# Performance work log

Measured on AMD Instinct MI355X. Metric: run time of the kernel, lower is better.

Reference implementation:

```python
import jax, jax.numpy as jnp
import numpy as np

EPS = 1e-6
ROPE_THETA = 1000000.0

def _rmsnorm(x, scale):
    var = jnp.mean(jnp.square(x), axis=-1, keepdims=True)
    return x * jax.lax.rsqrt(var + EPS) * scale

def _rope(x, positions):
    # x: [B, h, T, H]; GPT-NeoX style rotate-half
    H = x.shape[-1]
    half = H // 2
    inv_freq = 1.0 / (ROPE_THETA ** (jnp.arange(half, dtype=jnp.float32) * 2.0 / H))
    ang = positions.astype(jnp.float32)[:, None] * inv_freq[None, :]  # [T, half]
    cos, sin = jnp.cos(ang), jnp.sin(ang)
    x1, x2 = x[..., :half], x[..., half:]
    return jnp.concatenate([x1 * cos - x2 * sin, x2 * cos + x1 * sin], axis=-1)

def setup_inputs() -> dict:
    key = jax.random.key(0)
    ks = jax.random.split(key, 16)
    B, T, D = 2, 2048, 2048
    N, K, H = 16, 2, 128
    I = 5504
    s = 0.02
    return {
        "x": jax.random.normal(ks[0], (B, T, D), jnp.float32),
        "positions": jnp.arange(T, dtype=jnp.int32),
        "ln1_scale": jnp.ones((D,), jnp.float32),
        "q_w": jax.random.normal(ks[1], (N, D, H), jnp.float32) * s,
        "q_b": jax.random.normal(ks[2], (N, H), jnp.float32) * s,
        "k_w": jax.random.normal(ks[3], (K, D, H), jnp.float32) * s,
        "k_b": jax.random.normal(ks[4], (K, H), jnp.float32) * s,
        "v_w": jax.random.normal(ks[5], (K, D, H), jnp.float32) * s,
        "v_b": jax.random.normal(ks[6], (K, H), jnp.float32) * s,
        "o_w": jax.random.normal(ks[7], (N, H, D), jnp.float32) * s,
        "ln2_scale": jnp.ones((D,), jnp.float32),
        "gate_w": jax.random.normal(ks[8], (D, I), jnp.float32) * s,
        "up_w": jax.random.normal(ks[9], (D, I), jnp.float32) * s,
        "down_w": jax.random.normal(ks[10], (I, D), jnp.float32) * s,
    }

def reference(x, positions, ln1_scale, q_w, q_b, k_w, k_b, v_w, v_b, o_w,
              ln2_scale, gate_w, up_w, down_w):
    B, T, D = x.shape
    N, _, H = q_w.shape
    K = k_w.shape[0]
    group = N // K

    h = _rmsnorm(x, ln1_scale)

    # Projections (per source einsums) + bias
    q = jnp.einsum('btd,ndh->bnth', h, q_w) + q_b[None, :, None, :]
    k = jnp.einsum('btd,kdh->bkth', h, k_w) + k_b[None, :, None, :]
    v = jnp.einsum('btd,kdh->bkth', h, v_w) + v_b[None, :, None, :]

    q = _rope(q, positions) * (H ** -0.5)
    k = _rope(k, positions)

    # GQA: expand kv heads to query heads
    k = jnp.repeat(k, group, axis=1)  # [B,N,T,H]
    v = jnp.repeat(v, group, axis=1)

    # Causal self-attention (prefill path: kv cache filled from k, v)
    scores = jnp.einsum('bnth,bnsh->bnts', q, k)
    causal = positions[:, None] >= positions[None, :]  # [T, T]
    scores = jnp.where(causal[None, None, :, :], scores, -jnp.inf)
    probs = jax.nn.softmax(scores, axis=-1)
    attn = jnp.einsum('bnts,bnsh->bnth', probs, v)

    o = jnp.einsum('bnth,nhd->btd', attn, o_w)

    # Residual + post-attn norm + SwiGLU MLP + residual
    res = o + x
    h2 = _rmsnorm(res, ln2_scale)
    fuse = jax.nn.silu(h2 @ gate_w) * (h2 @ up_w)
    return res + fuse @ down_w
```

## Files before the change

### kernel.cpp

```cpp
#include <hip/hip_runtime.h>
#include <cstdint>
#include <cstddef>

typedef unsigned short u16;
typedef __attribute__((ext_vector_type(8))) short short8;
typedef __attribute__((ext_vector_type(4))) float f32x4;

#define DEV __device__ __forceinline__

DEV float bf2f(u16 v) { union { unsigned u; float f; } x; x.u = ((unsigned)v) << 16; return x.f; }
DEV u16 f2bf(float f) {
  union { float f; unsigned u; } x; x.f = f;
  unsigned r = x.u + 0x7fffu + ((x.u >> 16) & 1u);
  return (u16)(r >> 16);
}

DEV void gload_lds16(const void* g, void* l) {
  __builtin_amdgcn_global_load_lds((const __attribute__((address_space(1))) void*)g,
                                   (__attribute__((address_space(3))) void*)l, 16, 0, 0);
}

#define BARRIER __builtin_amdgcn_s_barrier()
#define VM0 asm volatile("s_waitcnt vmcnt(0)" ::: "memory")
#define VM4 asm volatile("s_waitcnt vmcnt(4)" ::: "memory")

DEV void rmsnorm_row(const float* __restrict__ x, const float* __restrict__ scale,
                     u16* __restrict__ out, int row, int tid, float* red)
{
  const float* xr = x + (size_t)row * 2048;
  const float4 v0 = *(const float4*)&xr[tid * 8];
  const float4 v1 = *(const float4*)&xr[tid * 8 + 4];
  float ss = v0.x * v0.x + v0.y * v0.y + v0.z * v0.z + v0.w * v0.w +
             v1.x * v1.x + v1.y * v1.y + v1.z * v1.z + v1.w * v1.w;
#pragma unroll
  for (int d = 32; d > 0; d >>= 1) ss += __shfl_down(ss, d);
  if ((tid & 63) == 0) red[tid >> 6] = ss;
  __syncthreads();
  const float tot = red[0] + red[1] + red[2] + red[3];
  const float inv = rsqrtf(tot * (1.f / 2048.f) + 1e-6f);
  const float* sc = scale + tid * 8;
  short8 ov;
  ov[0] = (short)f2bf(v0.x * inv * sc[0]); ov[1] = (short)f2bf(v0.y * inv * sc[1]);
  ov[2] = (short)f2bf(v0.z * inv * sc[2]); ov[3] = (short)f2bf(v0.w * inv * sc[3]);
  ov[4] = (short)f2bf(v1.x * inv * sc[4]); ov[5] = (short)f2bf(v1.y * inv * sc[5]);
  ov[6] = (short)f2bf(v1.z * inv * sc[6]); ov[7] = (short)f2bf(v1.w * inv * sc[7]);
  *(short8*)&out[(size_t)row * 2048 + tid * 8] = ov;
}

DEV void transpose_tile(const float* __restrict__ in, u16* __restrict__ out,
                        int R, int C, int mode, int bx, int by, int bz,
                        int tid, float (&tile)[64][65])
{
  const int tx = tid & 31, ty = tid >> 5;
  const int c0 = bx * 64, r0 = by * 64;
  const float* inb = in + (size_t)bz * R * C;
  u16* outb = out + (size_t)bz * R * C;
#pragma unroll
  for (int i = 0; i < 8; ++i) {
    const int r = ty + i * 8;
    const float2 v = *(const float2*)&inb[(size_t)(r0 + r) * C + c0 + tx * 2];
    tile[r][tx * 2] = v.x;
    tile[r][tx * 2 + 1] = v.y;
  }
  __syncthreads();
#pragma unroll
  for (int i = 0; i < 8; ++i) {
    const int jj = ty + i * 8;
    const int j = c0 + jj;
    const int prow = mode ? ((j >> 7) * 256 + (((j >> 5) & 3) << 6) + ((mode == 2) << 5) + (j & 31))
                          : j;
    const unsigned a = f2bf(tile[tx * 2][jj]);
    const unsigned b = f2bf(tile[tx * 2 + 1][jj]);
    *(unsigned*)&outb[(size_t)prow * R + r0 + tx * 2] = a | (b << 16);
  }
}

__global__ __launch_bounds__(256) void prep_kernel(
    const float* __restrict__ q_w, const float* __restrict__ k_w,
    const float* __restrict__ v_w, const float* __restrict__ o_w,
    const float* __restrict__ gate_w, const float* __restrict__ up_w,
    const float* __restrict__ down_w,
    const float* __restrict__ qb, const float* __restrict__ kb,
    const float* __restrict__ vb,
    const float* __restrict__ x, const float* __restrict__ ln1,
    u16* __restrict__ wqkv_t, u16* __restrict__ o_wt,
    u16* __restrict__ gu_t, u16* __restrict__ d_t, float* __restrict__ bias,
    u16* __restrict__ hbuf)
{
  __shared__ float tile[64][65];
  const int bid = (int)blockIdx.x;
  const int tid = threadIdx.x;
  if (bid < 1024) {
    transpose_tile(q_w, wqkv_t, 2048, 128, 0, bid & 1, (bid >> 1) & 31, bid >> 6, tid, tile);
  } else if (bid < 1152) {
    const int l = bid - 1024;
    transpose_tile(k_w, wqkv_t + 2048LL * 2048, 2048, 128, 0, l & 1, (l >> 1) & 31, l >> 6, tid, tile);
  } else if (bid < 1280) {
    const int l = bid - 1152;
    transpose_tile(v_w, wqkv_t + 2304LL * 2048, 2048, 128, 0, l & 1, (l >> 1) & 31, l >> 6, tid, tile);
  } else if (bid < 2304) {
    const int l = bid - 1280;
    transpose_tile(o_w, o_wt, 2048, 2048, 0, l & 31, l >> 5, 0, tid, tile);
  } else if (bid < 5056) {
    const int l = bid - 2304;
    transpose_tile(gate_w, gu_t, 2048, 5504, 1, l % 86, l / 86, 0, tid, tile);
  } else if (bid < 7808) {
    const int l = bid - 5056;
    transpose_tile(up_w, gu_t, 2048, 5504, 2, l % 86, l / 86, 0, tid, tile);
  } else if (bid < 10560) {
    const int l = bid - 7808;
    transpose_tile(down_w, d_t, 5504, 2048, 0, l & 31, l >> 5, 0, tid, tile);
  } else if (bid < 10570) {
    const int i = (bid - 10560) * 256 + tid;
    if (i < 2048) bias[i] = qb[i];
    else if (i < 2304) bias[i] = kb[i - 2048];
    else if (i < 2560) bias[i] = vb[i - 2304];
  } else {
    rmsnorm_row(x, ln1, hbuf, bid - 10570, tid, &tile[0][0]);
  }
}

__global__ __launch_bounds__(256) void rmsnorm_kernel(
    const float* __restrict__ x, const float* __restrict__ scale, u16* __restrict__ out)
{
  __shared__ float red[4];
  rmsnorm_row(x, scale, out, blockIdx.x, threadIdx.x, red);
}

template <int BM, int BN, int TB, int MODE, int GR>
__global__ __launch_bounds__(TB, 512 / TB) void gemm_conv_kernel(
    const u16* __restrict__ A, const u16* __restrict__ Bt,
    void* C, const float* __restrict__ aux, int N, int K, int lda, int ldb)
{
  constexpr int MFRAG = BM / 32;
  constexpr int AISS = BM * 8 / TB;
  constexpr int BISS = BN * 8 / TB;
  constexpr int WN = BN / 64;
  __shared__ __align__(16) u16 As[2][BM * 64];
  __shared__ __align__(16) u16 Bs[3][BN * 64];

  const int tid = threadIdx.x;
  const int wv = tid >> 6, lane = tid & 63, lo = lane & 15, hi = lane >> 4;
  const int wm = wv / WN, wn = wv % WN;

  const int nwg = (int)gridDim.x;
  const int id0 = (int)blockIdx.x;
  const int id = (id0 & 7) * (nwg >> 3) + (id0 >> 3);
  const int ncol = N / BN;
  const int rg = id % GR, cc = (id / GR) % ncol, gg = id / (GR * ncol);
  const int by = gg * GR + rg, bx = cc;
  const int row0 = by * BM, col0 = bx * BN;

  const f32x4 fz = {0.f, 0.f, 0.f, 0.f};
  f32x4 acc[MFRAG][4];
#pragma unroll
  for (int m = 0; m < MFRAG; ++m)
#pragma unroll
    for (int n = 0; n < 4; ++n) acc[m][n] = fz;

  const int nt = K >> 6;

  auto STAGE_A = [&](int kt, int ab) {
#pragma unroll
    for (int i = 0; i < AISS; ++i) {
      const int f = i * TB + tid;
      const int rp = f >> 3, sp = tid & 7;
      gload_lds16(A + (size_t)(row0 + rp) * lda + kt * 64 + ((sp ^ (rp & 7)) * 8),
                  (char*)&As[ab][0] + (i * TB + wv * 64) * 16);
    }
  };
  auto STAGE_B = [&](int kt, int bb) {
#pragma unroll
    for (int i = 0; i < BISS; ++i) {
      const int f = i * TB + tid;
      const int rp = f >> 3, sp = tid & 7;
      gload_lds16(Bt + (size_t)(col0 + rp) * ldb + kt * 64 + ((sp ^ (rp & 7)) * 8),
                  (char*)&Bs[bb][0] + (i * TB + wv * 64) * 16);
    }
  };

#define LDA8M(ARR, BUF, S, G)                                                    \
  _Pragma("unroll")                                                              \
  for (int mt = 0; mt < 4; ++mt) {                                               \
    const int r = wm * (BM / 2) + ((G) * 4 + mt) * 16 + lo;                      \
    ARR[mt] = *(const short8*)&As[BUF][r * 64 + (((S) * 4 + hi) ^ (r & 7)) * 8]; \
  }
#define LDB8M(ARR, BUF, S)                                                       \
  _Pragma("unroll")                                                              \
  for (int nn = 0; nn < 4; ++nn) {                                               \
    const int r = wn * 64 + nn * 16 + lo;                                        \
    ARR[nn] = *(const short8*)&Bs[BUF][r * 64 + (((S) * 4 + hi) ^ (r & 7)) * 8]; \
  }
#define MFMA16M(AR, BR, G)                                                       \
  __builtin_amdgcn_s_setprio(1);                                                 \
  _Pragma("unroll")                                                              \
  for (int mt = 0; mt < 4; ++mt)                                                 \
    _Pragma("unroll")                                                            \
    for (int nn = 0; nn < 4; ++nn)                                               \
      acc[(G) * 4 + mt][nn] = __builtin_amdgcn_mfma_f32_16x16x32_bf16(           \
          AR[mt], BR[nn], acc[(G) * 4 + mt][nn], 0, 0, 0);                       \
  __builtin_amdgcn_s_setprio(0);

  STAGE_A(0, 0); STAGE_B(0, 0); STAGE_B(1, 1);
  VM4; BARRIER;

  int ab = 0, bcur = 0;
  for (int t = 0; t < nt; ++t) {
    const bool preA = (t + 1 < nt);
    const bool preB = (t + 2 < nt);
    const int bs2 = (bcur >= 1) ? bcur - 1 : 2;
    if constexpr (BM == 256) {
      short8 a0[4], a1[4], b0[4], a2[4], a3[4], b1[4];
      LDA8M(a0, ab, 0, 0); LDA8M(a1, ab, 0, 1); LDB8M(b0, bcur, 0);
      LDA8M(a2, ab, 1, 0); LDA8M(a3, ab, 1, 1); LDB8M(b1, bcur, 1);
      if (preA) STAGE_A(t + 1, ab ^ 1);
      if (preB) STAGE_B(t + 2, bs2);
      MFMA16M(a0, b0, 0); MFMA16M(a1, b0, 1);
      MFMA16M(a2, b1, 0); MFMA16M(a3, b1, 1);
      if (preA) { if (preB) VM4; else VM0; }
      BARRIER;
    } else {
      short8 a0[4], b0[4], a1[4], b1[4];
      LDA8M(a0, ab, 0, 0); LDB8M(b0, bcur, 0);
      LDA8M(a1, ab, 1, 0); LDB8M(b1, bcur, 1);
      if (preA) STAGE_A(t + 1, ab ^ 1);
      if (preB) STAGE_B(t + 2, bs2);
      MFMA16M(a0, b0, 0);
      MFMA16M(a1, b1, 0);
      if (preA) { if (preB) VM4; else VM0; }
      BARRIER;
    }
    ab ^= 1;
    bcur = (bcur == 2) ? 0 : bcur + 1;
  }
#undef LDA8M
#undef LDB8M
#undef MFMA16M

  float* Cf = (float*)C;
  u16* Ch = (u16*)C;
  if constexpr (MODE == 4) {
    const int ldo = N >> 1;
#pragma unroll
    for (int fm = 0; fm < MFRAG; ++fm) {
#pragma unroll
      for (int nn = 0; nn < 2; ++nn) {
        const int fcol = (col0 >> 1) + wn * 32 + nn * 16 + lo;
#pragma unroll
        for (int j = 0; j < 4; ++j) {
          const int row = row0 + wm * (BM / 2) + fm * 16 + hi * 4 + j;
          const float g = acc[fm][nn][j];
          const float u = acc[fm][nn + 2][j];
          const float sg = g / (1.f + __builtin_amdgcn_exp2f(-1.4426950408889634f * g));
          Ch[(size_t)row * ldo + fcol] = f2bf(sg * u);
        }
      }
    }
  } else {
#pragma unroll
    for (int fm = 0; fm < MFRAG; ++fm) {
#pragma unroll
      for (int nn = 0; nn < 4; ++nn) {
        const int col = col0 + wn * 64 + nn * 16 + lo;
#pragma unroll
        for (int j = 0; j < 4; ++j) {
          const int row = row0 + wm * (BM / 2) + fm * 16 + hi * 4 + j;
          const size_t idx = (size_t)row * N + col;
          const float v = acc[fm][nn][j];
          if (MODE == 0) Cf[idx] = v + aux[col];
          else if (MODE == 1) Cf[idx] = v + aux[idx];
          else if (MODE == 2) Ch[idx] = f2bf(v);
          else Ch[idx] = f2bf(v + aux[col]);
        }
      }
    }
  }
}

__global__ __launch_bounds__(256) void rope_qkv_kernel(
    const u16* __restrict__ qkv, const int* __restrict__ pos,
    u16* __restrict__ Qb, u16* __restrict__ Kb, u16* __restrict__ Vt)
{
  const int idx = blockIdx.x * 256 + threadIdx.x;
  const int bt = idx / 1408;
  const int r = idx - bt * 1408;
  const int t = bt & 2047, b = bt >> 11;
  if (r < 1152) {
    const bool isq = r < 1024;
    const int rr = isq ? r : r - 1024;
    const int n = rr >> 6, hp = rr & 63;
    const u16* q = qkv + (size_t)bt * 2560 + (isq ? 0 : 2048) + n * 128 + hp;
    const float x1 = bf2f(q[0]);
    const float x2 = bf2f(q[64]);
    const float inv = exp2f((float)hp * (-19.931568569324174f / 64.f));
    const float ang = (float)pos[t] * inv;
    float s, c;
    sincosf(ang, &s, &c);
    const float sc = isq ? 0.08838834764831845f * 1.4426950408889634f : 1.f;
    const size_t base = isq ? (((size_t)(b * 16 + n) * 2048 + t) * 128 + hp)
                            : (((size_t)(b * 2 + n) * 2048 + t) * 128 + hp);
    u16* outp = isq ? Qb : Kb;
    outp[base] = f2bf((x1 * c - x2 * s) * sc);
    outp[base + 64] = f2bf((x2 * c + x1 * s) * sc);
  } else {
    const int rr = r - 1152;
    const int kh = rr >> 7, hh = rr & 127;
    Vt[((size_t)((b * 2 + kh) * 128 + hh)) * 2048 + t] =
        qkv[(size_t)bt * 2560 + 2304 + kh * 128 + hh];
  }
}

__global__ __launch_bounds__(512) void attn_kernel(
    const u16* __restrict__ Qb, const u16* __restrict__ Kb,
    const u16* __restrict__ Vt, u16* __restrict__ Out)
{
  __shared__ u16 Ks[2][128 * 128];
  __shared__ u16 Vs[2][128 * 128];
  __shared__ u16 Ps[8][16 * 128];
  const int tid = threadIdx.x;
  const int wave = tid >> 6, lane = tid & 63, lo = lane & 15, hi = lane >> 4;
  const int bn = blockIdx.x;
  const int b = bn >> 4, n = bn & 15, kh = n >> 3;

  const f32x4 fz = {0.f, 0.f, 0.f, 0.f};
  const u16* kg = Kb + (size_t)(b * 2 + kh) * 2048 * 128;
  const u16* vg = Vt + (size_t)(b * 2 + kh) * 128 * 2048;

  auto STAGE = [&](int buf, int s0) {
#pragma unroll
    for (int i = 0; i < 4; ++i) {
      const int gk = i * 512 + tid;
      const int rk = gk >> 4, gck = gk & 15;
      gload_lds16(kg + (size_t)(s0 + rk) * 128 + ((gck ^ (rk & 7)) * 8),
                  (char*)&Ks[buf][0] + (i * 512 + wave * 64) * 16);
      gload_lds16(vg + (size_t)rk * 2048 + s0 + ((gck ^ (rk & 7)) * 8),
                  (char*)&Vs[buf][0] + (i * 512 + wave * 64) * 16);
    }
  };

  auto processTile = [&](int q0) {
    const int nblk = q0 / 128 + 1;
    const u16* qptr = Qb + ((size_t)((b * 16 + n) * 2048) + q0 + wave * 16 + lo) * 128;
    short8 qf[4];
#pragma unroll
    for (int kc = 0; kc < 4; ++kc) qf[kc] = *(const short8*)&qptr[kc * 32 + hi * 8];

    float m_r[4], l_r[4];
    f32x4 oacc[8];
#pragma unroll
    for (int j = 0; j < 4; ++j) { m_r[j] = -1e30f; l_r[j] = 0.f; }
#pragma unroll
    for (int ht = 0; ht < 8; ++ht) oacc[ht] = fz;

    __syncthreads();
    STAGE(0, 0);
    __syncthreads();

    int cur = 0;
    for (int sb = 0; sb < nblk; ++sb) {
      const int s0 = sb * 128;
      if (sb + 1 < nblk) STAGE(cur ^ 1, s0 + 128);

      float sall[8][4];
      __builtin_amdgcn_s_setprio(1);
#pragma unroll
      for (int st = 0; st < 8; ++st) {
        f32x4 s = fz;
#pragma unroll
        for (int kc = 0; kc < 4; ++kc) {
          const int row = st * 16 + lo;
          const int cb = (kc * 64 + hi * 16) ^ ((lo & 7) << 4);
          short8 kf = *(const short8*)&Ks[cur][row * 128 + (cb >> 1)];
          s = __builtin_amdgcn_mfma_f32_16x16x32_bf16(qf[kc], kf, s, 0, 0, 0);
        }
#pragma unroll
        for (int j = 0; j < 4; ++j) sall[st][j] = s[j];
      }
      __builtin_amdgcn_s_setprio(0);

      if (s0 + 128 > q0) {
#pragma unroll
        for (int st = 0; st < 8; ++st) {
          const int sg = s0 + st * 16 + lo;
#pragma unroll
          for (int j = 0; j < 4; ++j) {
            const int qg = q0 + wave * 16 + hi * 4 + j;
            if (sg > qg) sall[st][j] = -1e30f;
          }
        }
      }

      float tmax[4];
#pragma unroll
      for (int j = 0; j < 4; ++j) {
        float t = fmaxf(fmaxf(fmaxf(sall[0][j], sall[1][j]), fmaxf(sall[2][j], sall[3][j])),
                        fmaxf(fmaxf(sall[4][j], sall[5][j]), fmaxf(sall[6][j], sall[7][j])));
        t = fmaxf(t, __shfl_xor(t, 1));
        t = fmaxf(t, __shfl_xor(t, 2));
        t = fmaxf(t, __shfl_xor(t, 4));
        t = fmaxf(t, __shfl_xor(t, 8));
        tmax[j] = t;
      }
      const bool defer = __all((tmax[0] - m_r[0] <= 8.f) & (tmax[1] - m_r[1] <= 8.f) &
                               (tmax[2] - m_r[2] <= 8.f) & (tmax[3] - m_r[3] <= 8.f));
      if (!defer) {
        float alpha[4];
#pragma unroll
        for (int j = 0; j < 4; ++j) {
          const float mnew = fmaxf(m_r[j], tmax[j]);
          alpha[j] = __builtin_amdgcn_exp2f(m_r[j] - mnew);
          m_r[j] = mnew;
          l_r[j] *= alpha[j];
        }
#pragma unroll
        for (int ht = 0; ht < 8; ++ht) {
#pragma unroll
          for (int j = 0; j < 4; ++j) oacc[ht][j] *= alpha[j];
        }
      }

      float rsum[4] = {0.f, 0.f, 0.f, 0.f};
#pragma unroll
      for (int st = 0; st < 8; ++st) {
#pragma unroll
        for (int j = 0; j < 4; ++j) {
          const float p = __builtin_amdgcn_exp2f(sall[st][j] - m_r[j]);
          rsum[j] += p;
          const int row = hi * 4 + j;
          const int cbp = (st * 32 + lo * 2) ^ ((row & 7) << 4);
          Ps[wave][row * 128 + (cbp >> 1)] = f2bf(p);
        }
      }
#pragma unroll
      for (int j = 0; j < 4; ++j) {
        float rs = rsum[j];
        rs += __shfl_xor(rs, 1);
        rs += __shfl_xor(rs, 2);
        rs += __shfl_xor(rs, 4);
        rs += __shfl_xor(rs, 8);
        l_r[j] += rs;
      }

      asm volatile("s_waitcnt lgkmcnt(0)" ::: "memory");
      __builtin_amdgcn_sched_barrier(0);

      short8 pf[4];
#pragma unroll
      for (int s = 0; s < 4; ++s) {
        const int pcb = (s * 64 + hi * 16) ^ ((lo & 7) << 4);
        pf[s] = *(const short8*)&Ps[wave][lo * 128 + (pcb >> 1)];
      }
      __builtin_amdgcn_s_setprio(1);
#pragma unroll
      for (int ht = 0; ht < 8; ++ht) {
        const int row = ht * 16 + lo;
#pragma unroll
        for (int s = 0; s < 4; ++s) {
          const int cb = (s * 64 + hi * 16) ^ ((row & 7) << 4);
          const short8 vf = *(const short8*)&Vs[cur][row * 128 + (cb >> 1)];
          oacc[ht] = __builtin_amdgcn_mfma_f32_16x16x32_bf16(pf[s], vf, oacc[ht], 0, 0, 0);
        }
      }
      __builtin_amdgcn_s_setprio(0);

      if (sb + 1 < nblk) __syncthreads();
      cur ^= 1;
    }

#pragma unroll
    for (int j = 0; j < 4; ++j) {
      const float inv = 1.0f / l_r[j];
      const int trow = q0 + wave * 16 + hi * 4 + j;
      const size_t base = ((size_t)(b * 2048 + trow)) * 2048 + n * 128;
#pragma unroll
      for (int ht = 0; ht < 8; ++ht)
        Out[base + ht * 16 + lo] = f2bf(oacc[ht][j] * inv);
    }
  };

  processTile((int)(15 - blockIdx.y) * 128);
  processTile((int)blockIdx.y * 128);
}

extern "C" void kernel_launch(void* const* d_in, const int* in_sizes, int n_in,
                              void* d_out, int out_size, void* d_ws, size_t ws_size,
                              hipStream_t stream)
{
  const float* x      = (const float*)d_in[0];
  const int*   pos    = (const int*)d_in[1];
  const float* ln1    = (const float*)d_in[2];
  const float* q_w    = (const float*)d_in[3];
  const float* q_b    = (const float*)d_in[4];
  const float* k_w    = (const float*)d_in[5];
  const float* k_b    = (const float*)d_in[6];
  const float* v_w    = (const float*)d_in[7];
  const float* v_b    = (const float*)d_in[8];
  const float* o_w    = (const float*)d_in[9];
  const float* ln2    = (const float*)d_in[10];
  const float* gate_w = (const float*)d_in[11];
  const float* up_w   = (const float*)d_in[12];
  const float* down_w = (const float*)d_in[13];
  float* out = (float*)d_out;

  char* w = (char*)d_ws;
  u16* wqkv_t = (u16*)w;       w += 2560LL * 2048 * 2;
  u16* o_wt   = (u16*)w;       w += 2048LL * 2048 * 2;
  u16* gu_t   = (u16*)w;       w += 11008LL * 2048 * 2;
  u16* d_t    = (u16*)w;       w += 2048LL * 5504 * 2;
  u16* hbuf   = (u16*)w;       w += 4096LL * 2048 * 2;
  float* bias_qkv = (float*)w; w += 2560 * 4;
  char* un = w;
  u16*  qkv   = (u16*)un;
  u16*  Qb    = (u16*)(un + 41943040LL);
  u16*  Kb    = (u16*)(un + 41943040LL + 16777216LL);
  u16*  Vt    = (u16*)(un + 41943040LL + 16777216LL + 2097152LL);
  u16*  attnb = (u16*)(un + 41943040LL + 16777216LL + 2097152LL + 2097152LL);
  u16*  fusebuf = (u16*)un;

  prep_kernel<<<14666, 256, 0, stream>>>(q_w, k_w, v_w, o_w, gate_w, up_w, down_w,
                                         q_b, k_b, v_b, x, ln1,
                                         wqkv_t, o_wt, gu_t, d_t, bias_qkv, hbuf);

  gemm_conv_kernel<128, 128, 256, 3, 8><<<640, 256, 0, stream>>>(hbuf, wqkv_t, qkv, bias_qkv, 2560, 2048, 2048, 2048);
  rope_qkv_kernel<<<22528, 256, 0, stream>>>(qkv, pos, Qb, Kb, Vt);
  attn_kernel<<<dim3(32, 8), 512, 0, stream>>>(Qb, Kb, Vt, attnb);
  gemm_conv_kernel<128, 128, 256, 1, 8><<<512, 256, 0, stream>>>(attnb, o_wt, out, x, 2048, 2048, 2048, 2048);
  rmsnorm_kernel<<<4096, 256, 0, stream>>>(out, ln2, hbuf);
  gemm_conv_kernel<256, 256, 512, 4, 4><<<688, 512, 0, stream>>>(hbuf, gu_t, fusebuf, nullptr, 11008, 2048, 2048, 2048);
  gemm_conv_kernel<128, 128, 256, 1, 8><<<512, 256, 0, stream>>>(fusebuf, d_t, out, out, 2048, 5504, 5504, 5504);
}
```

Baseline: 506.7 us.

## Overlap MLP weight transposes with QKV GEMM in a combined kernel

The gate/up/down weight transpose-to-bf16 work moves out of the prep kernel into a new kernel whose first 640 blocks run the QKV projection GEMM and whose remaining blocks do the transposes. The memory-bound transpose traffic is meant to overlap with the compute-bound GEMM, and the prep kernel shrinks. The GEMM is a hardcoded copy of the MODE 3 path, and the transpose blocks reuse the GEMM's LDS buffer as their tile, so the combined kernel carries the larger LDS footprint. Block scheduling order may leave the GEMM blocks competing with the transposes or finishing last.

Measured after the change: 517.2 us. +2.1%, slower.

```diff
diff --git a/kernel.cpp b/kernel.cpp
--- a/kernel.cpp
+++ b/kernel.cpp
@@ -78,14 +78,11 @@
 __global__ __launch_bounds__(256) void prep_kernel(
     const float* __restrict__ q_w, const float* __restrict__ k_w,
     const float* __restrict__ v_w, const float* __restrict__ o_w,
-    const float* __restrict__ gate_w, const float* __restrict__ up_w,
-    const float* __restrict__ down_w,
     const float* __restrict__ qb, const float* __restrict__ kb,
     const float* __restrict__ vb,
     const float* __restrict__ x, const float* __restrict__ ln1,
     u16* __restrict__ wqkv_t, u16* __restrict__ o_wt,
-    u16* __restrict__ gu_t, u16* __restrict__ d_t, float* __restrict__ bias,
-    u16* __restrict__ hbuf)
+    float* __restrict__ bias, u16* __restrict__ hbuf)
 {
   __shared__ float tile[64][65];
   const int bid = (int)blockIdx.x;
@@ -101,22 +98,13 @@
   } else if (bid < 2304) {
     const int l = bid - 1280;
     transpose_tile(o_w, o_wt, 2048, 2048, 0, l & 31, l >> 5, 0, tid, tile);
-  } else if (bid < 5056) {
-    const int l = bid - 2304;
-    transpose_tile(gate_w, gu_t, 2048, 5504, 1, l % 86, l / 86, 0, tid, tile);
-  } else if (bid < 7808) {
-    const int l = bid - 5056;
-    transpose_tile(up_w, gu_t, 2048, 5504, 2, l % 86, l / 86, 0, tid, tile);
-  } else if (bid < 10560) {
-    const int l = bid - 7808;
-    transpose_tile(down_w, d_t, 5504, 2048, 0, l & 31, l >> 5, 0, tid, tile);
-  } else if (bid < 10570) {
-    const int i = (bid - 10560) * 256 + tid;
+  } else if (bid < 2314) {
+    const int i = (bid - 2304) * 256 + tid;
     if (i < 2048) bias[i] = qb[i];
     else if (i < 2304) bias[i] = kb[i - 2048];
     else if (i < 2560) bias[i] = vb[i - 2304];
   } else {
-    rmsnorm_row(x, ln1, hbuf, bid - 10570, tid, &tile[0][0]);
+    rmsnorm_row(x, ln1, hbuf, bid - 2314, tid, &tile[0][0]);
   }
 }
 
@@ -125,6 +113,135 @@
 {
   __shared__ float red[4];
   rmsnorm_row(x, scale, out, blockIdx.x, threadIdx.x, red);
+}
+
+__global__ __launch_bounds__(256, 2) void qkv_prep2_kernel(
+    const u16* __restrict__ A, const u16* __restrict__ Bt,
+    u16* __restrict__ C, const float* __restrict__ aux,
+    const float* __restrict__ gate_w, const float* __restrict__ up_w,
+    const float* __restrict__ down_w,
+    u16* __restrict__ gu_t, u16* __restrict__ d_t)
+{
+  constexpr int BM = 128, BN = 128, TB = 256, GR = 8;
+  constexpr int MFRAG = 4, AISS = 4, BISS = 4, WN = 2;
+  constexpr int NGEMM = 640;
+  const int N = 2560, K = 2048, lda = 2048, ldb = 2048;
+  __shared__ __align__(16) u16 As[2][BM * 64];
+  __shared__ __align__(16) u16 Bs[3][BN * 64];
+
+  const int tid = threadIdx.x;
+  const int bid = (int)blockIdx.x;
+
+  if (bid >= NGEMM) {
+    auto& tile = *reinterpret_cast<float(*)[64][65]>(&As[0][0]);
+    const int l = bid - NGEMM;
+    if (l < 2752) {
+      transpose_tile(gate_w, gu_t, 2048, 5504, 1, l % 86, l / 86, 0, tid, tile);
+    } else if (l < 5504) {
+      const int m = l - 2752;
+      transpose_tile(up_w, gu_t, 2048, 5504, 2, m % 86, m / 86, 0, tid, tile);
+    } else {
+      const int m = l - 5504;
+      transpose_tile(down_w, d_t, 5504, 2048, 0, m & 31, m >> 5, 0, tid, tile);
+    }
+    return;
+  }
+
+  const int wv = tid >> 6, lane = tid & 63, lo = lane & 15, hi = lane >> 4;
+  const int wm = wv / WN, wn = wv % WN;
+
+  const int id = (bid & 7) * (NGEMM >> 3) + (bid >> 3);
+  const int ncol = N / BN;
+  const int rg = id % GR, cc = (id / GR) % ncol, gg = id / (GR * ncol);
+  const int by = gg * GR + rg, bx = cc;
+  const int row0 = by * BM, col0 = bx * BN;
+
+  const f32x4 fz = {0.f, 0.f, 0.f, 0.f};
+  f32x4 acc[MFRAG][4];
+#pragma unroll
+  for (int m = 0; m < MFRAG; ++m)
+#pragma unroll
+    for (int n = 0; n < 4; ++n) acc[m][n] = fz;
+
+  const int nt = K >> 6;
+
+  auto STAGE_A = [&](int kt, int ab) {
+#pragma unroll
+    for (int i = 0; i < AISS; ++i) {
+      const int f = i * TB + tid;
+      const int rp = f >> 3, sp = tid & 7;
+      gload_lds16(A + (size_t)(row0 + rp) * lda + kt * 64 + ((sp ^ (rp & 7)) * 8),
+                  (char*)&As[ab][0] + (i * TB + wv * 64) * 16);
+    }
+  };
+  auto STAGE_B = [&](int kt, int bb) {
+#pragma unroll
+    for (int i = 0; i < BISS; ++i) {
+      const int f = i * TB + tid;
+      const int rp = f >> 3, sp = tid & 7;
+      gload_lds16(Bt + (size_t)(col0 + rp) * ldb + kt * 64 + ((sp ^ (rp & 7)) * 8),
+                  (char*)&Bs[bb][0] + (i * TB + wv * 64) * 16);
+    }
+  };
+
+#define LDA8Q(ARR, BUF, S, G)                                                    \
+  _Pragma("unroll")                                                              \
+  for (int mt = 0; mt < 4; ++mt) {                                               \
+    const int r = wm * (BM / 2) + ((G) * 4 + mt) * 16 + lo;                      \
+    ARR[mt] = *(const short8*)&As[BUF][r * 64 + (((S) * 4 + hi) ^ (r & 7)) * 8]; \
+  }
+#define LDB8Q(ARR, BUF, S)                                                       \
+  _Pragma("unroll")                                                              \
+  for (int nn = 0; nn < 4; ++nn) {                                               \
+    const int r = wn * 64 + nn * 16 + lo;                                        \
+    ARR[nn] = *(const short8*)&Bs[BUF][r * 64 + (((S) * 4 + hi) ^ (r & 7)) * 8]; \
+  }
+#define MFMA16Q(AR, BR, G)                                                       \
+  __builtin_amdgcn_s_setprio(1);                                                 \
+  _Pragma("unroll")                                                              \
+  for (int mt = 0; mt < 4; ++mt)                                                 \
+    _Pragma("unroll")                                                            \
+    for (int nn = 0; nn < 4; ++nn)                                               \
+      acc[(G) * 4 + mt][nn] = __builtin_amdgcn_mfma_f32_16x16x32_bf16(           \
+          AR[mt], BR[nn], acc[(G) * 4 + mt][nn], 0, 0, 0);                       \
+  __builtin_amdgcn_s_setprio(0);
+
+  STAGE_A(0, 0); STAGE_B(0, 0); STAGE_B(1, 1);
+  VM4; BARRIER;
+
+  int ab = 0, bcur = 0;
+  for (int t = 0; t < nt; ++t) {
+    const bool preA = (t + 1 < nt);
+    const bool preB = (t + 2 < nt);
+    const int bs2 = (bcur >= 1) ? bcur - 1 : 2;
+    short8 a0[4], b0[4], a1[4], b1[4];
+    LDA8Q(a0, ab, 0, 0); LDB8Q(b0, bcur, 0);
+    LDA8Q(a1, ab, 1, 0); LDB8Q(b1, bcur, 1);
+    if (preA) STAGE_A(t + 1, ab ^ 1);
+    if (preB) STAGE_B(t + 2, bs2);
+    MFMA16Q(a0, b0, 0);
+    MFMA16Q(a1, b1, 0);
+    if (preA) { if (preB) VM4; else VM0; }
+    BARRIER;
+    ab ^= 1;
+    bcur = (bcur == 2) ? 0 : bcur + 1;
+  }
+#undef LDA8Q
+#undef LDB8Q
+#undef MFMA16Q
+
+#pragma unroll
+  for (int fm = 0; fm < MFRAG; ++fm) {
+#pragma unroll
+    for (int nn = 0; nn < 4; ++nn) {
+      const int col = col0 + wn * 64 + nn * 16 + lo;
+#pragma unroll
+      for (int j = 0; j < 4; ++j) {
+        const int row = row0 + wm * (BM / 2) + fm * 16 + hi * 4 + j;
+        C[(size_t)row * N + col] = f2bf(acc[fm][nn][j] + aux[col]);
+      }
+    }
+  }
 }
 
 template <int BM, int BN, int TB, int MODE, int GR>
@@ -517,11 +634,12 @@
   u16*  attnb = (u16*)(un + 41943040LL + 16777216LL + 2097152LL + 2097152LL);
   u16*  fusebuf = (u16*)un;
 
-  prep_kernel<<<14666, 256, 0, stream>>>(q_w, k_w, v_w, o_w, gate_w, up_w, down_w,
-                                         q_b, k_b, v_b, x, ln1,
-                                         wqkv_t, o_wt, gu_t, d_t, bias_qkv, hbuf);
-
-  gemm_conv_kernel<128, 128, 256, 3, 8><<<640, 256, 0, stream>>>(hbuf, wqkv_t, qkv, bias_qkv, 2560, 2048, 2048, 2048);
+  prep_kernel<<<6410, 256, 0, stream>>>(q_w, k_w, v_w, o_w, q_b, k_b, v_b,
+                                        x, ln1, wqkv_t, o_wt, bias_qkv, hbuf);
+
+  qkv_prep2_kernel<<<8896, 256, 0, stream>>>(hbuf, wqkv_t, qkv, bias_qkv,
+                                             gate_w, up_w, down_w, gu_t, d_t);
+
   rope_qkv_kernel<<<22528, 256, 0, stream>>>(qkv, pos, Qb, Kb, Vt);
   attn_kernel<<<dim3(32, 8), 512, 0, stream>>>(Qb, Kb, Vt, attnb);
   gemm_conv_kernel<128, 128, 256, 1, 8><<<512, 256, 0, stream>>>(attnb, o_wt, out, x, 2048, 2048, 2048, 2048);
```
